# Kernel tuning notes

Hardware: AMD Instinct MI355X
Metric: run time of the kernel (lower is better)

The kernel has to match this reference:

```python
import jax, jax.numpy as jnp
import numpy as np

# ---- FBPinn configuration (matches init_kwargs) ----
NW = 16            # nwindows
NEUR = 32          # neurons
DOM = (0.0, 1.0)   # domain
OVERLAP = 0.25
SIGMA = 0.005
U_MEAN = 0.0
U_SD = 1.0
OMEGA = 15.0       # hard constraint: tanh(omega*x) * pred
WIN_THRESH = 1e-5

# ---- static subdomain geometry (partition_domain / get_midpoints) ----
def _geometry():
    w = (DOM[1] - DOM[0]) / NW
    sub = np.zeros((NW, 2), dtype=np.float64)
    for i in range(NW):
        sub[i, 0] = DOM[0] if i == 0 else DOM[0] + (i - OVERLAP / 2) * w
        sub[i, 1] = DOM[1] if i == NW - 1 else DOM[0] + (i + 1 + OVERLAP / 2) * w
    means = (sub[:, 1] + sub[:, 0]) / 2
    std = (sub[:, 1] - sub[:, 0]) / 2
    mo = np.zeros(NW + 1, dtype=np.float64)  # overlap midpoints
    mo[0] = sub[0, 0]
    mo[NW] = sub[NW - 1, 1]
    mo[1:NW] = (sub[:-1, 1] + sub[1:, 0]) / 2
    return means.astype(np.float32), std.astype(np.float32), mo.astype(np.float32)

MEANS, STD, MO = _geometry()


def setup_inputs() -> dict:
    key = jax.random.key(0)
    kx, k1, k2, k3 = jax.random.split(key, 4)
    N = 2097152
    x = jax.random.uniform(kx, (N,), dtype=jnp.float32)  # points in [0,1) = domain
    # stacked per-window MLP params: 1 -> NEUR -> NEUR -> 1, tanh
    s1 = 1.0                      # fan_in = 1
    s2 = 1.0 / np.sqrt(NEUR)
    W1 = jax.random.normal(k1, (NW, 1, NEUR), dtype=jnp.float32) * s1
    b1 = jnp.zeros((NW, NEUR), dtype=jnp.float32)
    W2 = jax.random.normal(k2, (NW, NEUR, NEUR), dtype=jnp.float32) * s2
    b2 = jnp.zeros((NW, NEUR), dtype=jnp.float32)
    W3 = jax.random.normal(k3, (NW, NEUR, 1), dtype=jnp.float32) * s2
    b3 = jnp.zeros((NW, 1), dtype=jnp.float32)
    return {"x": x, "W1": W1, "b1": b1, "W2": W2, "b2": b2, "W3": W3, "b3": b3}


def reference(x, W1, b1, W2, b2, W3, b3):
    # FBPinn.forward: sum over windows of (window weight * per-window MLP output),
    # masked to window support (window > 1e-5), then hard constraint.
    pred = jnp.zeros_like(x)
    for i in range(NW):  # fixed small window count
        win = jax.nn.sigmoid((x - MO[i]) / SIGMA) * jax.nn.sigmoid(-(x - MO[i + 1]) / SIGMA)
        mask = win > WIN_THRESH
        xn = (x - MEANS[i]) / STD[i]                 # subdomain normalization
        h = jnp.tanh(xn[:, None] * W1[i][0] + b1[i])  # [N, NEUR]
        h = jnp.tanh(h @ W2[i] + b2[i])               # [N, NEUR]
        out = (h @ W3[i])[:, 0] + b3[i][0]            # [N]
        out = out * U_SD + U_MEAN                     # unnormalize
        pred = pred + jnp.where(mask, win * out, 0.0) # masked scatter-add
    pred = jnp.tanh(OMEGA * x) * pred                 # hard constraint
    return pred
```

## Files before the change

### kernel.cpp

```cpp
#include <hip/hip_runtime.h>
#include <math.h>

#define NW 16
#define NEUR 32
#define TTAB 8192
#define WSUB 0.0625f
#define INV_SIGMA 200.0f
#define OMEGA 15.0f
#define WTHRESH 1e-5f
#define EVAL_BLOCKS 512
#define EVAL_THREADS 256

__device__ __forceinline__ float sigmoid_f(float z) {
    return 1.0f / (1.0f + __expf(-z));
}
__device__ __forceinline__ float tanh_fast(float z) {
    const float e = __expf(2.0f * z);
    return 1.0f - 2.0f / (e + 1.0f);
}

__global__ __launch_bounds__(256) void build_F(
    const float* __restrict__ W1, const float* __restrict__ b1,
    const float* __restrict__ W2, const float* __restrict__ b2,
    const float* __restrict__ W3, const float* __restrict__ b3,
    float* __restrict__ partial) {
    const int d = blockIdx.y;
    const int g = blockIdx.x * blockDim.x + threadIdx.x;

    const float x = (float)g * (1.0f / (float)(TTAB - 1));
    int i0 = (int)(x * 16.0f);
    if (i0 > NW - 1) i0 = NW - 1;
    const int c = i0 - 1 + d;

    float val = 0.0f;
    if (c >= 0 && c < NW) {
        const float s1 = sigmoid_f((x - (float)c * WSUB) * INV_SIGMA);
        const float s2 = sigmoid_f(-(x - (float)(c + 1) * WSUB) * INV_SIGMA);
        const float win = s1 * s2;
        if (win > WTHRESH) {
            float mean, sd;
            if (c == 0)            { mean = 0.03515625f; sd = 0.03515625f; }
            else if (c == NW - 1)  { mean = 0.96484375f; sd = 0.03515625f; }
            else                   { mean = ((float)c + 0.5f) * 0.0625f; sd = 0.0390625f; }
            const float xn = (x - mean) / sd;

            const float* __restrict__ W1c = W1 + c * NEUR;
            const float* __restrict__ b1c = b1 + c * NEUR;
            float h1[NEUR];
#pragma unroll
            for (int j = 0; j < NEUR; ++j)
                h1[j] = tanh_fast(fmaf(xn, W1c[j], b1c[j]));

            const float* __restrict__ W2c = W2 + c * NEUR * NEUR;
            const float* __restrict__ b2c = b2 + c * NEUR;
            float h2[NEUR];
#pragma unroll
            for (int j = 0; j < NEUR; ++j) h2[j] = b2c[j];
#pragma unroll 4
            for (int k = 0; k < NEUR; ++k) {
                const float hk = h1[k];
                const float4* __restrict__ row = (const float4*)(W2c + k * NEUR);
#pragma unroll
                for (int q = 0; q < NEUR / 4; ++q) {
                    const float4 wv = row[q];
                    h2[q * 4 + 0] = fmaf(hk, wv.x, h2[q * 4 + 0]);
                    h2[q * 4 + 1] = fmaf(hk, wv.y, h2[q * 4 + 1]);
                    h2[q * 4 + 2] = fmaf(hk, wv.z, h2[q * 4 + 2]);
                    h2[q * 4 + 3] = fmaf(hk, wv.w, h2[q * 4 + 3]);
                }
            }

            const float* __restrict__ W3c = W3 + c * NEUR;
            float acc = b3[c];
#pragma unroll
            for (int k = 0; k < NEUR; ++k)
                acc = fmaf(tanh_fast(h2[k]), W3c[k], acc);

            val = win * acc;
        }
    }
    partial[d * TTAB + g] = val;
}

__global__ __launch_bounds__(EVAL_THREADS) void eval_F(
    const float* __restrict__ x, const float* __restrict__ partial,
    float* __restrict__ out, int n) {
    __shared__ float F[TTAB];

    {
        const float4* __restrict__ p = (const float4*)partial;
        float4* Fv = (float4*)F;
        const int Q = TTAB / 4;
#pragma unroll
        for (int i = threadIdx.x; i < Q; i += EVAL_THREADS) {
            const float4 a = p[i];
            const float4 b = p[i + Q];
            const float4 c = p[i + 2 * Q];
            float4 r;
            r.x = a.x + b.x + c.x;
            r.y = a.y + b.y + c.y;
            r.z = a.z + b.z + c.z;
            r.w = a.w + b.w + c.w;
            Fv[i] = r;
        }
    }
    __syncthreads();

    const int n4 = n >> 2;
    const int stride = gridDim.x * blockDim.x;
    for (int idx = blockIdx.x * blockDim.x + threadIdx.x; idx < n4; idx += stride) {
        const float4 xv = *(const float4*)(x + idx * 4);
        float4 r;
#pragma unroll
        for (int e = 0; e < 4; ++e) {
            const float xe = (&xv.x)[e];
            float t = xe * (float)(TTAB - 1);
            t = fminf(fmaxf(t, 0.0f), (float)(TTAB - 1) - 0.5f);
            const int it = (int)t;
            const float f = t - (float)it;
            const float u0 = F[it];
            const float u1 = F[it + 1];
            const float u = fmaf(f, u1 - u0, u0);
            (&r.x)[e] = tanh_fast(OMEGA * xe) * u;
        }
        *(float4*)(out + idx * 4) = r;
    }
    if (blockIdx.x == 0) {
        const int tail = n & 3;
        if ((int)threadIdx.x < tail) {
            const float xe = x[n4 * 4 + threadIdx.x];
            float t = xe * (float)(TTAB - 1);
            t = fminf(fmaxf(t, 0.0f), (float)(TTAB - 1) - 0.5f);
            const int it = (int)t;
            const float f = t - (float)it;
            const float u = fmaf(f, F[it + 1] - F[it], F[it]);
            out[n4 * 4 + threadIdx.x] = tanh_fast(OMEGA * xe) * u;
        }
    }
}

extern "C" void kernel_launch(void* const* d_in, const int* in_sizes, int n_in,
                              void* d_out, int out_size, void* d_ws, size_t ws_size,
                              hipStream_t stream) {
    const float* x  = (const float*)d_in[0];
    const float* W1 = (const float*)d_in[1];
    const float* b1 = (const float*)d_in[2];
    const float* W2 = (const float*)d_in[3];
    const float* b2 = (const float*)d_in[4];
    const float* W3 = (const float*)d_in[5];
    const float* b3 = (const float*)d_in[6];
    float* out = (float*)d_out;
    float* partial = (float*)d_ws;
    const int n = in_sizes[0];

    build_F<<<dim3(TTAB / 256, 3), 256, 0, stream>>>(W1, b1, W2, b2, W3, b3, partial);
    eval_F<<<EVAL_BLOCKS, EVAL_THREADS, 0, stream>>>(x, partial, out, n);
}
```

Before: 102.0 us.

## Fuse table build and evaluation into one cooperative kernel with grid sync

Merges the lookup-table build kernel and the evaluation kernel into a single cooperative launch. Each block computes 16 table nodes (three window terms each), reduces them in shared memory, writes them to workspace, and then a grid-wide sync lets every block copy the full table into LDS before interpolating. The aim is to drop one kernel launch and the three-way partial-sum readback. In exchange it adds grid-sync overhead and cooperative-launch constraints, and only 48 threads per block do the MLP work, which leaves most lanes idle during the build phase.

Result: slower. 143.5 us (+40.7%).

```diff
diff --git a/kernel.cpp b/kernel.cpp
--- a/kernel.cpp
+++ b/kernel.cpp
@@ -1,5 +1,8 @@
 #include <hip/hip_runtime.h>
+#include <hip/hip_cooperative_groups.h>
 #include <math.h>
+
+namespace cg = cooperative_groups;
 
 #define NW 16
 #define NEUR 32
@@ -8,8 +11,9 @@
 #define INV_SIGMA 200.0f
 #define OMEGA 15.0f
 #define WTHRESH 1e-5f
-#define EVAL_BLOCKS 512
-#define EVAL_THREADS 256
+#define BLOCKS 512
+#define THREADS 256
+#define NODES_PER_BLOCK (TTAB / BLOCKS)
 
 __device__ __forceinline__ float sigmoid_f(float z) {
     return 1.0f / (1.0f + __expf(-z));
@@ -19,105 +23,104 @@
     return 1.0f - 2.0f / (e + 1.0f);
 }
 
-__global__ __launch_bounds__(256) void build_F(
+__device__ float window_term(float x, int c,
+                             const float* __restrict__ W1, const float* __restrict__ b1,
+                             const float* __restrict__ W2, const float* __restrict__ b2,
+                             const float* __restrict__ W3, const float* __restrict__ b3) {
+    if (c < 0 || c >= NW) return 0.0f;
+    const float s1 = sigmoid_f((x - (float)c * WSUB) * INV_SIGMA);
+    const float s2 = sigmoid_f(-(x - (float)(c + 1) * WSUB) * INV_SIGMA);
+    const float win = s1 * s2;
+    if (win <= WTHRESH) return 0.0f;
+
+    float mean, sd;
+    if (c == 0)            { mean = 0.03515625f; sd = 0.03515625f; }
+    else if (c == NW - 1)  { mean = 0.96484375f; sd = 0.03515625f; }
+    else                   { mean = ((float)c + 0.5f) * 0.0625f; sd = 0.0390625f; }
+    const float xn = (x - mean) / sd;
+
+    const float* __restrict__ W1c = W1 + c * NEUR;
+    const float* __restrict__ b1c = b1 + c * NEUR;
+    float h1[NEUR];
+#pragma unroll
+    for (int j = 0; j < NEUR; ++j)
+        h1[j] = tanh_fast(fmaf(xn, W1c[j], b1c[j]));
+
+    const float* __restrict__ W2c = W2 + c * NEUR * NEUR;
+    const float* __restrict__ b2c = b2 + c * NEUR;
+    float h2[NEUR];
+#pragma unroll
+    for (int j = 0; j < NEUR; ++j) h2[j] = b2c[j];
+#pragma unroll 4
+    for (int k = 0; k < NEUR; ++k) {
+        const float hk = h1[k];
+        const float4* __restrict__ row = (const float4*)(W2c + k * NEUR);
+#pragma unroll
+        for (int q = 0; q < NEUR / 4; ++q) {
+            const float4 wv = row[q];
+            h2[q * 4 + 0] = fmaf(hk, wv.x, h2[q * 4 + 0]);
+            h2[q * 4 + 1] = fmaf(hk, wv.y, h2[q * 4 + 1]);
+            h2[q * 4 + 2] = fmaf(hk, wv.z, h2[q * 4 + 2]);
+            h2[q * 4 + 3] = fmaf(hk, wv.w, h2[q * 4 + 3]);
+        }
+    }
+
+    const float* __restrict__ W3c = W3 + c * NEUR;
+    float acc = b3[c];
+#pragma unroll
+    for (int k = 0; k < NEUR; ++k)
+        acc = fmaf(tanh_fast(h2[k]), W3c[k], acc);
+
+    return win * acc;
+}
+
+__global__ __launch_bounds__(THREADS) void fbpinn_fused(
+    const float* __restrict__ x,
     const float* __restrict__ W1, const float* __restrict__ b1,
     const float* __restrict__ W2, const float* __restrict__ b2,
     const float* __restrict__ W3, const float* __restrict__ b3,
-    float* __restrict__ partial) {
-    const int d = blockIdx.y;
-    const int g = blockIdx.x * blockDim.x + threadIdx.x;
-
-    const float x = (float)g * (1.0f / (float)(TTAB - 1));
-    int i0 = (int)(x * 16.0f);
-    if (i0 > NW - 1) i0 = NW - 1;
-    const int c = i0 - 1 + d;
-
-    float val = 0.0f;
-    if (c >= 0 && c < NW) {
-        const float s1 = sigmoid_f((x - (float)c * WSUB) * INV_SIGMA);
-        const float s2 = sigmoid_f(-(x - (float)(c + 1) * WSUB) * INV_SIGMA);
-        const float win = s1 * s2;
-        if (win > WTHRESH) {
-            float mean, sd;
-            if (c == 0)            { mean = 0.03515625f; sd = 0.03515625f; }
-            else if (c == NW - 1)  { mean = 0.96484375f; sd = 0.03515625f; }
-            else                   { mean = ((float)c + 0.5f) * 0.0625f; sd = 0.0390625f; }
-            const float xn = (x - mean) / sd;
-
-            const float* __restrict__ W1c = W1 + c * NEUR;
-            const float* __restrict__ b1c = b1 + c * NEUR;
-            float h1[NEUR];
-#pragma unroll
-            for (int j = 0; j < NEUR; ++j)
-                h1[j] = tanh_fast(fmaf(xn, W1c[j], b1c[j]));
-
-            const float* __restrict__ W2c = W2 + c * NEUR * NEUR;
-            const float* __restrict__ b2c = b2 + c * NEUR;
-            float h2[NEUR];
-#pragma unroll
-            for (int j = 0; j < NEUR; ++j) h2[j] = b2c[j];
-#pragma unroll 4
-            for (int k = 0; k < NEUR; ++k) {
-                const float hk = h1[k];
-                const float4* __restrict__ row = (const float4*)(W2c + k * NEUR);
-#pragma unroll
-                for (int q = 0; q < NEUR / 4; ++q) {
-                    const float4 wv = row[q];
-                    h2[q * 4 + 0] = fmaf(hk, wv.x, h2[q * 4 + 0]);
-                    h2[q * 4 + 1] = fmaf(hk, wv.y, h2[q * 4 + 1]);
-                    h2[q * 4 + 2] = fmaf(hk, wv.z, h2[q * 4 + 2]);
-                    h2[q * 4 + 3] = fmaf(hk, wv.w, h2[q * 4 + 3]);
-                }
-            }
-
-            const float* __restrict__ W3c = W3 + c * NEUR;
-            float acc = b3[c];
-#pragma unroll
-            for (int k = 0; k < NEUR; ++k)
-                acc = fmaf(tanh_fast(h2[k]), W3c[k], acc);
-
-            val = win * acc;
-        }
-    }
-    partial[d * TTAB + g] = val;
-}
-
-__global__ __launch_bounds__(EVAL_THREADS) void eval_F(
-    const float* __restrict__ x, const float* __restrict__ partial,
-    float* __restrict__ out, int n) {
+    float* __restrict__ F_ws, float* __restrict__ out, int n) {
     __shared__ float F[TTAB];
 
+    const int t = threadIdx.x;
+    if (t < 3 * NODES_PER_BLOCK) {
+        const int node_local = t / 3;
+        const int d = t - 3 * node_local;
+        const int g = blockIdx.x * NODES_PER_BLOCK + node_local;
+        const float xg = (float)g * (1.0f / (float)(TTAB - 1));
+        int i0 = (int)(xg * 16.0f);
+        if (i0 > NW - 1) i0 = NW - 1;
+        F[t] = window_term(xg, i0 - 1 + d, W1, b1, W2, b2, W3, b3);
+    }
+    __syncthreads();
+    if (t < NODES_PER_BLOCK) {
+        const float s = F[3 * t] + F[3 * t + 1] + F[3 * t + 2];
+        F_ws[blockIdx.x * NODES_PER_BLOCK + t] = s;
+    }
+
+    cg::this_grid().sync();
+
     {
-        const float4* __restrict__ p = (const float4*)partial;
-        float4* Fv = (float4*)F;
-        const int Q = TTAB / 4;
+        const float4* __restrict__ src = (const float4*)F_ws;
+        float4* dst = (float4*)F;
 #pragma unroll
-        for (int i = threadIdx.x; i < Q; i += EVAL_THREADS) {
-            const float4 a = p[i];
-            const float4 b = p[i + Q];
-            const float4 c = p[i + 2 * Q];
-            float4 r;
-            r.x = a.x + b.x + c.x;
-            r.y = a.y + b.y + c.y;
-            r.z = a.z + b.z + c.z;
-            r.w = a.w + b.w + c.w;
-            Fv[i] = r;
-        }
+        for (int i = t; i < TTAB / 4; i += THREADS)
+            dst[i] = src[i];
     }
     __syncthreads();
 
     const int n4 = n >> 2;
     const int stride = gridDim.x * blockDim.x;
-    for (int idx = blockIdx.x * blockDim.x + threadIdx.x; idx < n4; idx += stride) {
+    for (int idx = blockIdx.x * blockDim.x + t; idx < n4; idx += stride) {
         const float4 xv = *(const float4*)(x + idx * 4);
         float4 r;
 #pragma unroll
         for (int e = 0; e < 4; ++e) {
             const float xe = (&xv.x)[e];
-            float t = xe * (float)(TTAB - 1);
-            t = fminf(fmaxf(t, 0.0f), (float)(TTAB - 1) - 0.5f);
-            const int it = (int)t;
-            const float f = t - (float)it;
+            float tt = xe * (float)(TTAB - 1);
+            tt = fminf(fmaxf(tt, 0.0f), (float)(TTAB - 1) - 0.5f);
+            const int it = (int)tt;
+            const float f = tt - (float)it;
             const float u0 = F[it];
             const float u1 = F[it + 1];
             const float u = fmaf(f, u1 - u0, u0);
@@ -127,14 +130,14 @@
     }
     if (blockIdx.x == 0) {
         const int tail = n & 3;
-        if ((int)threadIdx.x < tail) {
-            const float xe = x[n4 * 4 + threadIdx.x];
-            float t = xe * (float)(TTAB - 1);
-            t = fminf(fmaxf(t, 0.0f), (float)(TTAB - 1) - 0.5f);
-            const int it = (int)t;
-            const float f = t - (float)it;
+        if (t < tail) {
+            const float xe = x[n4 * 4 + t];
+            float tt = xe * (float)(TTAB - 1);
+            tt = fminf(fmaxf(tt, 0.0f), (float)(TTAB - 1) - 0.5f);
+            const int it = (int)tt;
+            const float f = tt - (float)it;
             const float u = fmaf(f, F[it + 1] - F[it], F[it]);
-            out[n4 * 4 + threadIdx.x] = tanh_fast(OMEGA * xe) * u;
+            out[n4 * 4 + t] = tanh_fast(OMEGA * xe) * u;
         }
     }
 }
@@ -150,9 +153,11 @@
     const float* W3 = (const float*)d_in[5];
     const float* b3 = (const float*)d_in[6];
     float* out = (float*)d_out;
-    float* partial = (float*)d_ws;
-    const int n = in_sizes[0];
+    float* F_ws = (float*)d_ws;
+    int n = in_sizes[0];
 
-    build_F<<<dim3(TTAB / 256, 3), 256, 0, stream>>>(W1, b1, W2, b2, W3, b3, partial);
-    eval_F<<<EVAL_BLOCKS, EVAL_THREADS, 0, stream>>>(x, partial, out, n);
+    void* args[] = { (void*)&x, (void*)&W1, (void*)&b1, (void*)&W2, (void*)&b2,
+                     (void*)&W3, (void*)&b3, (void*)&F_ws, (void*)&out, (void*)&n };
+    hipLaunchCooperativeKernel((void*)fbpinn_fused, dim3(BLOCKS), dim3(THREADS),
+                               args, 0, stream);
 }
```
